# Optimization experiments

Measured on AMD Instinct MI355X. Metric: run time of the kernel, lower is better.

Reference implementation:

```python
import jax, jax.numpy as jnp
import numpy as np
from jax import lax

C = 256
K = 7
PAD = (K - 1) // 2
EMB = 128
MULT = 4
HID = C * MULT
B = 16
L = 4096
EPS = 1e-6
LAYER_SCALE_INIT = 1e-6


def setup_inputs() -> dict:
    key = jax.random.key(0)
    ks = jax.random.split(key, 10)
    x = jax.random.normal(ks[0], (B, C, L), dtype=jnp.float32)
    t = jax.random.normal(ks[1], (B, EMB), dtype=jnp.float32)
    # depthwise conv: Conv1d(C, C, K, groups=C) -> weight [C, 1, K]
    dw_w = jax.random.normal(ks[2], (C, 1, K), dtype=jnp.float32) * 0.1
    dw_b = jax.random.normal(ks[3], (C,), dtype=jnp.float32) * 0.02
    # FiLM linear: Linear(EMB, 2C)
    film_w = jax.random.normal(ks[4], (2 * C, EMB), dtype=jnp.float32) * 0.05
    film_b = jax.random.normal(ks[5], (2 * C,), dtype=jnp.float32) * 0.02
    # pointwise 1x1 convs
    pw1_w = jax.random.normal(ks[6], (HID, C), dtype=jnp.float32) * 0.05
    pw1_b = jax.random.normal(ks[7], (HID,), dtype=jnp.float32) * 0.02
    pw2_w = jax.random.normal(ks[8], (C, HID), dtype=jnp.float32) * 0.05
    pw2_b = jax.random.normal(ks[9], (C,), dtype=jnp.float32) * 0.02
    gamma = jnp.full((C, 1), LAYER_SCALE_INIT, dtype=jnp.float32)
    return {"x": x, "t": t, "dw_w": dw_w, "dw_b": dw_b,
            "film_w": film_w, "film_b": film_b,
            "pw1_w": pw1_w, "pw1_b": pw1_b,
            "pw2_w": pw2_w, "pw2_b": pw2_b, "gamma": gamma}


def reference(x, t, dw_w, dw_b, film_w, film_b, pw1_w, pw1_b, pw2_w, pw2_b, gamma):
    # circular pad on spatial dim, then valid depthwise conv
    xp = jnp.concatenate([x[..., -PAD:], x, x[..., :PAD]], axis=-1)  # [B, C, L+2*PAD]
    y = lax.conv_general_dilated(
        xp, dw_w, window_strides=(1,), padding='VALID',
        dimension_numbers=('NCH', 'OIH', 'NCH'),
        feature_group_count=C) + dw_b[:, None]                       # [B, C, L]
    # GroupNorm(1, C, affine=False): normalize over (C, L) per sample
    mu = jnp.mean(y, axis=(1, 2), keepdims=True)
    var = jnp.mean(jnp.square(y - mu), axis=(1, 2), keepdims=True)
    yn = (y - mu) * lax.rsqrt(var + EPS)
    # FiLM: scale/shift from embedded time
    ss = t @ film_w.T + film_b                                       # [B, 2C]
    scale, shift = jnp.split(ss, 2, axis=1)                          # [B, C] each
    yn = yn * (scale[:, :, None] + 1.0) + shift[:, :, None]
    # pointwise mixing with ReLU
    h = jax.nn.relu(jnp.einsum('bcl,dc->bdl', yn, pw1_w) + pw1_b[:, None])  # [B, HID, L]
    branch = jnp.einsum('bdl,cd->bcl', h, pw2_w) + pw2_b[:, None]           # [B, C, L]
    # layerscale + residual
    return x + branch * gamma
```

## Files before the change

kernel.cpp:

```cpp
#include <hip/hip_runtime.h>

typedef short s16x8 __attribute__((ext_vector_type(8)));
typedef short s16x4 __attribute__((ext_vector_type(4)));
typedef float f32x4 __attribute__((ext_vector_type(4)));

#define NB 16
#define NC 256
#define NL 4096
#define NH 1024
#define NE 128

#define WS_YNT   0ull
#define WS_PW1   33554432ull
#define WS_PW2   34078720ull
#define WS_AF    34603008ull
#define WS_BF    34619392ull

#define MFMA16(a, b, c) __builtin_amdgcn_mfma_f32_16x16x32_bf16((a), (b), (c), 0, 0, 0)

static __device__ __forceinline__ short f2bf(float f) {
    unsigned int u = __float_as_uint(f);
    u = (u + 0x7fffu + ((u >> 16) & 1u)) >> 16;
    return (short)u;
}
static __device__ __forceinline__ float bf2f(short s) {
    return __uint_as_float(((unsigned int)(unsigned short)s) << 16);
}

__global__ __launch_bounds__(256) void k0_prep(const float4* __restrict__ pw1,
                                               const float4* __restrict__ pw2,
                                               s16x4* __restrict__ pw1b,
                                               s16x4* __restrict__ pw2b) {
    const int idx = blockIdx.x * 256 + threadIdx.x;
    const float4 a = pw1[idx];
    const float4 b = pw2[idx];
    s16x4 oa, ob;
    oa[0] = f2bf(a.x); oa[1] = f2bf(a.y); oa[2] = f2bf(a.z); oa[3] = f2bf(a.w);
    ob[0] = f2bf(b.x); ob[1] = f2bf(b.y); ob[2] = f2bf(b.z); ob[3] = f2bf(b.w);
    pw1b[idx] = oa;
    pw2b[idx] = ob;
}

__global__ __launch_bounds__(256) void k1_dwconv(const float* __restrict__ x,
                                                 const float* __restrict__ dw_w,
                                                 const float* __restrict__ dw_b,
                                                 short* __restrict__ ynt,
                                                 float2* __restrict__ psum) {
    __shared__ float xt[64][81];
    __shared__ float red1[4], red2[4];
    const int b = blockIdx.x >> 8;
    const int rem = blockIdx.x & 255;
    const int c0 = (rem >> 6) << 6;
    const int l0 = (rem & 63) << 6;
    const int t = threadIdx.x;

    const float* xb = x + ((size_t)(b * NC + c0)) * NL;
    {
#pragma unroll
        for (int j = 0; j < 5; ++j) {
            const int idx = t + 256 * j;
            const int row = idx / 20;
            const int col = idx - row * 20;
            const int lg = (l0 - 4 + col * 4) & (NL - 1);
            const float4 v = *(const float4*)(xb + (size_t)row * NL + lg);
            xt[row][col * 4 + 0] = v.x;
            xt[row][col * 4 + 1] = v.y;
            xt[row][col * 4 + 2] = v.z;
            xt[row][col * 4 + 3] = v.w;
        }
    }

    const int c = t & 63;
    const int w = t >> 6;
    const float w0 = dw_w[(c0 + c) * 7 + 0], w1 = dw_w[(c0 + c) * 7 + 1],
                w2 = dw_w[(c0 + c) * 7 + 2], w3 = dw_w[(c0 + c) * 7 + 3],
                w4 = dw_w[(c0 + c) * 7 + 4], w5 = dw_w[(c0 + c) * 7 + 5],
                w6 = dw_w[(c0 + c) * 7 + 6];
    const float bb = dw_b[c0 + c];
    __syncthreads();

    float win0 = xt[c][w * 16 + 1], win1 = xt[c][w * 16 + 2], win2 = xt[c][w * 16 + 3],
          win3 = xt[c][w * 16 + 4], win4 = xt[c][w * 16 + 5], win5 = xt[c][w * 16 + 6],
          win6 = xt[c][w * 16 + 7];
    float s1 = 0.f, s2 = 0.f;
    short* yo = ynt + ((size_t)(b * NL + l0 + w * 16)) * NC + c0 + c;
#pragma unroll
    for (int i = 0; i < 16; ++i) {
        const float y = bb + w0 * win0 + w1 * win1 + w2 * win2 + w3 * win3 +
                        w4 * win4 + w5 * win5 + w6 * win6;
        s1 += y;
        s2 += y * y;
        yo[(size_t)i * NC] = f2bf(y);
        win0 = win1; win1 = win2; win2 = win3; win3 = win4; win4 = win5; win5 = win6;
        win6 = xt[c][w * 16 + i + 8];
    }
    for (int off = 32; off; off >>= 1) {
        s1 += __shfl_down(s1, off, 64);
        s2 += __shfl_down(s2, off, 64);
    }
    if ((t & 63) == 0) { red1[w] = s1; red2[w] = s2; }
    __syncthreads();
    if (t == 0) {
        psum[blockIdx.x] = make_float2(red1[0] + red1[1] + red1[2] + red1[3],
                                       red2[0] + red2[1] + red2[2] + red2[3]);
    }
}

__global__ __launch_bounds__(256) void k2_finalize(const float* __restrict__ tin,
                                                   const float* __restrict__ fw,
                                                   const float* __restrict__ fb,
                                                   const float2* __restrict__ psum,
                                                   float* __restrict__ afilm,
                                                   float* __restrict__ bfilm) {
    __shared__ float r1[4], r2[4];
    const int b = blockIdx.x;
    const int c = threadIdx.x;

    const float2 v = psum[b * 256 + c];
    float s1 = v.x, s2 = v.y;
    for (int off = 32; off; off >>= 1) {
        s1 += __shfl_down(s1, off, 64);
        s2 += __shfl_down(s2, off, 64);
    }
    if ((c & 63) == 0) { r1[c >> 6] = s1; r2[c >> 6] = s2; }
    __syncthreads();
    const float sum1 = r1[0] + r1[1] + r1[2] + r1[3];
    const float sum2 = r2[0] + r2[1] + r2[2] + r2[3];

    const float n = (float)(NC * NL);
    const float mu = sum1 / n;
    const float var = sum2 / n - mu * mu;
    const float rs = rsqrtf(var + 1e-6f);

    const f32x4* tv = (const f32x4*)(tin + b * NE);
    const f32x4* wA = (const f32x4*)(fw + (size_t)c * NE);
    const f32x4* wB = (const f32x4*)(fw + (size_t)(NC + c) * NE);
    float sc = 0.f, sh = 0.f;
#pragma unroll
    for (int e = 0; e < NE / 4; ++e) {
        f32x4 tq = tv[e], aq = wA[e], bq = wB[e];
        sc += tq[0] * aq[0] + tq[1] * aq[1] + tq[2] * aq[2] + tq[3] * aq[3];
        sh += tq[0] * bq[0] + tq[1] * bq[1] + tq[2] * bq[2] + tq[3] * bq[3];
    }
    sc += fb[c];
    sh += fb[NC + c];
    const float A = rs * (1.f + sc);
    afilm[b * NC + c] = A;
    bfilm[b * NC + c] = sh - mu * A;
}

__global__ __launch_bounds__(256, 2) void k3_gemm(
    const short* __restrict__ ynt, const short* __restrict__ pw1b,
    const short* __restrict__ pw2b, const float* __restrict__ pb1,
    const float* __restrict__ pb2, const float* __restrict__ afilm,
    const float* __restrict__ bfilm, const float* __restrict__ gamma,
    const float* __restrict__ x, float* __restrict__ out, int b0) {
    __shared__ short yn[64 * 264];
    __shared__ short hs[2][64 * 136];

    const int b = (blockIdx.x >> 6) + b0;
    const int l0 = (blockIdx.x & 63) << 6;
    const int t = threadIdx.x;
    const int lane = t & 63, wid = t >> 6;
    const int ln = lane & 15, quad = lane >> 4;

    {
        const int c8 = (t & 31) * 8;
        const int lrow = t >> 5;
        const f32x4 a0 = *(const f32x4*)(afilm + b * NC + c8);
        const f32x4 a1 = *(const f32x4*)(afilm + b * NC + c8 + 4);
        const f32x4 f0 = *(const f32x4*)(bfilm + b * NC + c8);
        const f32x4 f1 = *(const f32x4*)(bfilm + b * NC + c8 + 4);
        const short* ys = ynt + ((size_t)(b * NL + l0)) * NC + c8;
#pragma unroll
        for (int p = 0; p < 8; ++p) {
            const int l = p * 8 + lrow;
            s16x8 v = *(const s16x8*)(ys + (size_t)l * NC);
            s16x8 o;
#pragma unroll
            for (int j = 0; j < 4; ++j) {
                o[j]     = f2bf(a0[j] * bf2f(v[j])     + f0[j]);
                o[4 + j] = f2bf(a1[j] * bf2f(v[4 + j]) + f1[j]);
            }
            *(s16x8*)(yn + l * 264 + c8) = o;
        }
    }

    const short* A1b = pw1b + (size_t)(32 * wid + ln) * NC + quad * 8;
    const short* A2b = pw2b + (size_t)(64 * wid + ln) * NH + quad * 8;

    s16x8 a1p[16];
#pragma unroll
    for (int kk = 0; kk < 4; ++kk) {
        a1p[2 * kk + 0] = *(const s16x8*)(A1b + kk * 32);
        a1p[2 * kk + 1] = *(const s16x8*)(A1b + 16 * NC + kk * 32);
    }
    __syncthreads();
#pragma unroll
    for (int kk = 4; kk < 8; ++kk) {
        a1p[2 * kk + 0] = *(const s16x8*)(A1b + kk * 32);
        a1p[2 * kk + 1] = *(const s16x8*)(A1b + 16 * NC + kk * 32);
    }

    s16x8 a2p[16];
#pragma unroll
    for (int kk = 0; kk < 4; ++kk) {
#pragma unroll
        for (int m = 0; m < 4; ++m) {
            a2p[4 * kk + m] = *(const s16x8*)(A2b + m * 16 * NH + kk * 32);
        }
    }

    f32x4 acc1[2][4] = {};
#pragma unroll
    for (int kk = 0; kk < 8; ++kk) {
        const int kq = kk * 32 + quad * 8;
        s16x8 b0v = *(const s16x8*)(yn + (0 * 16 + ln) * 264 + kq);
        s16x8 b1v = *(const s16x8*)(yn + (1 * 16 + ln) * 264 + kq);
        s16x8 b2v = *(const s16x8*)(yn + (2 * 16 + ln) * 264 + kq);
        s16x8 b3v = *(const s16x8*)(yn + (3 * 16 + ln) * 264 + kq);
        acc1[0][0] = MFMA16(a1p[2 * kk], b0v, acc1[0][0]);
        acc1[0][1] = MFMA16(a1p[2 * kk], b1v, acc1[0][1]);
        acc1[0][2] = MFMA16(a1p[2 * kk], b2v, acc1[0][2]);
        acc1[0][3] = MFMA16(a1p[2 * kk], b3v, acc1[0][3]);
        acc1[1][0] = MFMA16(a1p[2 * kk + 1], b0v, acc1[1][0]);
        acc1[1][1] = MFMA16(a1p[2 * kk + 1], b1v, acc1[1][1]);
        acc1[1][2] = MFMA16(a1p[2 * kk + 1], b2v, acc1[1][2]);
        acc1[1][3] = MFMA16(a1p[2 * kk + 1], b3v, acc1[1][3]);
    }

    f32x4 acc2[4][4] = {};

#pragma unroll 1
    for (int ch = 0; ch < 7; ++ch) {
        const int dc0 = ch * 128;
        short* hw = &hs[ch & 1][0];
#pragma unroll
        for (int mf = 0; mf < 2; ++mf) {
            const int dbase = 32 * wid + mf * 16 + quad * 4;
            const f32x4 b1v = *(const f32x4*)(pb1 + dc0 + dbase);
#pragma unroll
            for (int nf = 0; nf < 4; ++nf) {
                const int l = nf * 16 + ln;
                s16x4 hv;
#pragma unroll
                for (int r = 0; r < 4; ++r) {
                    hv[r] = f2bf(fmaxf(acc1[mf][nf][r] + b1v[r], 0.f));
                }
                *(s16x4*)(hw + l * 136 + dbase) = hv;
            }
        }
        __syncthreads();
        const short* A1n = A1b + (size_t)(dc0 + 128) * NC;
#pragma unroll
        for (int kk = 0; kk < 4; ++kk) {
            a1p[2 * kk + 0] = *(const s16x8*)(A1n + kk * 32);
            a1p[2 * kk + 1] = *(const s16x8*)(A1n + 16 * NC + kk * 32);
        }
        const short* hr = &hs[ch & 1][0];
#pragma unroll
        for (int kk = 0; kk < 4; ++kk) {
            const int kq = kk * 32 + quad * 8;
            s16x8 h0 = *(const s16x8*)(hr + (0 * 16 + ln) * 136 + kq);
            s16x8 h1 = *(const s16x8*)(hr + (1 * 16 + ln) * 136 + kq);
            s16x8 h2 = *(const s16x8*)(hr + (2 * 16 + ln) * 136 + kq);
            s16x8 h3 = *(const s16x8*)(hr + (3 * 16 + ln) * 136 + kq);
            acc2[0][0] = MFMA16(a2p[4 * kk + 0], h0, acc2[0][0]);
            acc2[0][1] = MFMA16(a2p[4 * kk + 0], h1, acc2[0][1]);
            acc2[0][2] = MFMA16(a2p[4 * kk + 0], h2, acc2[0][2]);
            acc2[0][3] = MFMA16(a2p[4 * kk + 0], h3, acc2[0][3]);
            acc2[1][0] = MFMA16(a2p[4 * kk + 1], h0, acc2[1][0]);
            acc2[1][1] = MFMA16(a2p[4 * kk + 1], h1, acc2[1][1]);
            acc2[1][2] = MFMA16(a2p[4 * kk + 1], h2, acc2[1][2]);
            acc2[1][3] = MFMA16(a2p[4 * kk + 1], h3, acc2[1][3]);
            acc2[2][0] = MFMA16(a2p[4 * kk + 2], h0, acc2[2][0]);
            acc2[2][1] = MFMA16(a2p[4 * kk + 2], h1, acc2[2][1]);
            acc2[2][2] = MFMA16(a2p[4 * kk + 2], h2, acc2[2][2]);
            acc2[2][3] = MFMA16(a2p[4 * kk + 2], h3, acc2[2][3]);
            acc2[3][0] = MFMA16(a2p[4 * kk + 3], h0, acc2[3][0]);
            acc2[3][1] = MFMA16(a2p[4 * kk + 3], h1, acc2[3][1]);
            acc2[3][2] = MFMA16(a2p[4 * kk + 3], h2, acc2[3][2]);
            acc2[3][3] = MFMA16(a2p[4 * kk + 3], h3, acc2[3][3]);
        }
#pragma unroll
        for (int kk = 4; kk < 8; ++kk) {
            a1p[2 * kk + 0] = *(const s16x8*)(A1n + kk * 32);
            a1p[2 * kk + 1] = *(const s16x8*)(A1n + 16 * NC + kk * 32);
        }
        {
            const short* A2n = A2b + dc0 + 128;
#pragma unroll
            for (int kk = 0; kk < 4; ++kk) {
#pragma unroll
                for (int m = 0; m < 4; ++m) {
                    a2p[4 * kk + m] = *(const s16x8*)(A2n + m * 16 * NH + kk * 32);
                }
            }
        }
#pragma unroll
        for (int i = 0; i < 2; ++i)
#pragma unroll
            for (int j = 0; j < 4; ++j) acc1[i][j] = (f32x4){0.f, 0.f, 0.f, 0.f};
#pragma unroll
        for (int kk = 0; kk < 8; ++kk) {
            const int kq = kk * 32 + quad * 8;
            s16x8 b0v = *(const s16x8*)(yn + (0 * 16 + ln) * 264 + kq);
            s16x8 b1v = *(const s16x8*)(yn + (1 * 16 + ln) * 264 + kq);
            s16x8 b2v = *(const s16x8*)(yn + (2 * 16 + ln) * 264 + kq);
            s16x8 b3v = *(const s16x8*)(yn + (3 * 16 + ln) * 264 + kq);
            acc1[0][0] = MFMA16(a1p[2 * kk], b0v, acc1[0][0]);
            acc1[0][1] = MFMA16(a1p[2 * kk], b1v, acc1[0][1]);
            acc1[0][2] = MFMA16(a1p[2 * kk], b2v, acc1[0][2]);
            acc1[0][3] = MFMA16(a1p[2 * kk], b3v, acc1[0][3]);
            acc1[1][0] = MFMA16(a1p[2 * kk + 1], b0v, acc1[1][0]);
            acc1[1][1] = MFMA16(a1p[2 * kk + 1], b1v, acc1[1][1]);
            acc1[1][2] = MFMA16(a1p[2 * kk + 1], b2v, acc1[1][2]);
            acc1[1][3] = MFMA16(a1p[2 * kk + 1], b3v, acc1[1][3]);
        }
    }

    {
        short* hw = &hs[1][0];
#pragma unroll
        for (int mf = 0; mf < 2; ++mf) {
            const int dbase = 32 * wid + mf * 16 + quad * 4;
            const f32x4 b1v = *(const f32x4*)(pb1 + 7 * 128 + dbase);
#pragma unroll
            for (int nf = 0; nf < 4; ++nf) {
                const int l = nf * 16 + ln;
                s16x4 hv;
#pragma unroll
                for (int r = 0; r < 4; ++r) {
                    hv[r] = f2bf(fmaxf(acc1[mf][nf][r] + b1v[r], 0.f));
                }
                *(s16x4*)(hw + l * 136 + dbase) = hv;
            }
        }
        __syncthreads();
        const short* hr = &hs[1][0];
#pragma unroll
        for (int kk = 0; kk < 4; ++kk) {
            const int kq = kk * 32 + quad * 8;
            s16x8 h0 = *(const s16x8*)(hr + (0 * 16 + ln) * 136 + kq);
            s16x8 h1 = *(const s16x8*)(hr + (1 * 16 + ln) * 136 + kq);
            s16x8 h2 = *(const s16x8*)(hr + (2 * 16 + ln) * 136 + kq);
            s16x8 h3 = *(const s16x8*)(hr + (3 * 16 + ln) * 136 + kq);
            acc2[0][0] = MFMA16(a2p[4 * kk + 0], h0, acc2[0][0]);
            acc2[0][1] = MFMA16(a2p[4 * kk + 0], h1, acc2[0][1]);
            acc2[0][2] = MFMA16(a2p[4 * kk + 0], h2, acc2[0][2]);
            acc2[0][3] = MFMA16(a2p[4 * kk + 0], h3, acc2[0][3]);
            acc2[1][0] = MFMA16(a2p[4 * kk + 1], h0, acc2[1][0]);
            acc2[1][1] = MFMA16(a2p[4 * kk + 1], h1, acc2[1][1]);
            acc2[1][2] = MFMA16(a2p[4 * kk + 1], h2, acc2[1][2]);
            acc2[1][3] = MFMA16(a2p[4 * kk + 1], h3, acc2[1][3]);
            acc2[2][0] = MFMA16(a2p[4 * kk + 2], h0, acc2[2][0]);
            acc2[2][1] = MFMA16(a2p[4 * kk + 2], h1, acc2[2][1]);
            acc2[2][2] = MFMA16(a2p[4 * kk + 2], h2, acc2[2][2]);
            acc2[2][3] = MFMA16(a2p[4 * kk + 2], h3, acc2[2][3]);
            acc2[3][0] = MFMA16(a2p[4 * kk + 3], h0, acc2[3][0]);
            acc2[3][1] = MFMA16(a2p[4 * kk + 3], h1, acc2[3][1]);
            acc2[3][2] = MFMA16(a2p[4 * kk + 3], h2, acc2[3][2]);
            acc2[3][3] = MFMA16(a2p[4 * kk + 3], h3, acc2[3][3]);
        }
    }

#pragma unroll
    for (int mf2 = 0; mf2 < 4; ++mf2) {
        const int cbase = 64 * wid + mf2 * 16 + quad * 4;
        const f32x4 g4 = *(const f32x4*)(gamma + cbase);
        const f32x4 b4 = *(const f32x4*)(pb2 + cbase);
#pragma unroll
        for (int r = 0; r < 4; ++r) {
            const int c = cbase + r;
            const size_t base = ((size_t)(b * NC + c)) * NL + l0 + ln;
            const float* xr = x + base;
            float* orow = out + base;
#pragma unroll
            for (int nf2 = 0; nf2 < 4; ++nf2) {
                orow[nf2 * 16] = xr[nf2 * 16] + g4[r] * (acc2[mf2][nf2][r] + b4[r]);
            }
        }
    }
}

extern "C" void kernel_launch(void* const* d_in, const int* in_sizes, int n_in,
                              void* d_out, int out_size, void* d_ws, size_t ws_size,
                              hipStream_t stream) {
    (void)in_sizes; (void)n_in; (void)out_size; (void)ws_size;
    const float* x      = (const float*)d_in[0];
    const float* tin    = (const float*)d_in[1];
    const float* dw_w   = (const float*)d_in[2];
    const float* dw_b   = (const float*)d_in[3];
    const float* film_w = (const float*)d_in[4];
    const float* film_b = (const float*)d_in[5];
    const float* pw1_w  = (const float*)d_in[6];
    const float* pw1_b  = (const float*)d_in[7];
    const float* pw2_w  = (const float*)d_in[8];
    const float* pw2_b  = (const float*)d_in[9];
    const float* gamma  = (const float*)d_in[10];
    float* out = (float*)d_out;

    char* ws = (char*)d_ws;
    short* ynt  = (short*)(ws + WS_YNT);
    short* pw1b = (short*)(ws + WS_PW1);
    short* pw2b = (short*)(ws + WS_PW2);
    float* afilm = (float*)(ws + WS_AF);
    float* bfilm = (float*)(ws + WS_BF);
    float2* psum = (float2*)d_out;

    hipLaunchKernelGGL(k0_prep, dim3(256), dim3(256), 0, stream,
                       (const float4*)pw1_w, (const float4*)pw2_w,
                       (s16x4*)pw1b, (s16x4*)pw2b);
    hipLaunchKernelGGL(k1_dwconv, dim3(NB * 256), dim3(256), 0, stream,
                       x, dw_w, dw_b, ynt, psum);
    hipLaunchKernelGGL(k2_finalize, dim3(NB), dim3(256), 0, stream,
                       tin, film_w, film_b, psum, afilm, bfilm);
    hipLaunchKernelGGL(k3_gemm, dim3((NB / 4) * (NL / 64)), dim3(256), 0, stream,
                       ynt, pw1b, pw2b, pw1_b, pw2_b, afilm, bfilm, gamma, x, out, 0);
    hipLaunchKernelGGL(k3_gemm, dim3((NB / 4) * (NL / 64)), dim3(256), 0, stream,
                       ynt, pw1b, pw2b, pw1_b, pw2_b, afilm, bfilm, gamma, x, out, 4);
    hipLaunchKernelGGL(k3_gemm, dim3((NB / 4) * (NL / 64)), dim3(256), 0, stream,
                       ynt, pw1b, pw2b, pw1_b, pw2_b, afilm, bfilm, gamma, x, out, 8);
    hipLaunchKernelGGL(k3_gemm, dim3((NB / 4) * (NL / 64)), dim3(256), 0, stream,
                       ynt, pw1b, pw2b, pw1_b, pw2_b, afilm, bfilm, gamma, x, out, 12);
}
```

Measured before the change: 323.3 us.

## Fuse weight prep into dwconv and FiLM finalize into GEMM, single GEMM launch

Merges the bf16 weight conversion into the depthwise-conv kernel as extra blocks. It moves the GroupNorm/FiLM finalize into the start of every GEMM block, so each block recomputes the per-sample scale and shift into shared memory. The four per-batch-chunk GEMM launches become one launch over all batches, and psum moves from the output buffer into the workspace. This cuts the launch count from seven to two and removes the serial tiny finalize kernel. The cost is redundant FiLM dot products and reductions in each of the 1024 GEMM blocks, plus slightly more shared memory.

```diff
diff --git a/kernel.cpp b/kernel.cpp
--- a/kernel.cpp
+++ b/kernel.cpp
@@ -13,8 +13,7 @@
 #define WS_YNT   0ull
 #define WS_PW1   33554432ull
 #define WS_PW2   34078720ull
-#define WS_AF    34603008ull
-#define WS_BF    34619392ull
+#define WS_PSUM  34603008ull
 
 #define MFMA16(a, b, c) __builtin_amdgcn_mfma_f32_16x16x32_bf16((a), (b), (c), 0, 0, 0)
 
@@ -27,32 +26,35 @@
     return __uint_as_float(((unsigned int)(unsigned short)s) << 16);
 }
 
-__global__ __launch_bounds__(256) void k0_prep(const float4* __restrict__ pw1,
-                                               const float4* __restrict__ pw2,
-                                               s16x4* __restrict__ pw1b,
-                                               s16x4* __restrict__ pw2b) {
-    const int idx = blockIdx.x * 256 + threadIdx.x;
-    const float4 a = pw1[idx];
-    const float4 b = pw2[idx];
-    s16x4 oa, ob;
-    oa[0] = f2bf(a.x); oa[1] = f2bf(a.y); oa[2] = f2bf(a.z); oa[3] = f2bf(a.w);
-    ob[0] = f2bf(b.x); ob[1] = f2bf(b.y); ob[2] = f2bf(b.z); ob[3] = f2bf(b.w);
-    pw1b[idx] = oa;
-    pw2b[idx] = ob;
-}
-
-__global__ __launch_bounds__(256) void k1_dwconv(const float* __restrict__ x,
+__global__ __launch_bounds__(256) void k01_fused(const float* __restrict__ x,
                                                  const float* __restrict__ dw_w,
                                                  const float* __restrict__ dw_b,
                                                  short* __restrict__ ynt,
-                                                 float2* __restrict__ psum) {
+                                                 float2* __restrict__ psum,
+                                                 const float4* __restrict__ pw1,
+                                                 const float4* __restrict__ pw2,
+                                                 s16x4* __restrict__ pw1b,
+                                                 s16x4* __restrict__ pw2b) {
     __shared__ float xt[64][81];
     __shared__ float red1[4], red2[4];
+    const int t = threadIdx.x;
+
+    if (blockIdx.x >= NB * 256) {
+        const int idx = (blockIdx.x - NB * 256) * 256 + t;
+        const float4 a = pw1[idx];
+        const float4 bq = pw2[idx];
+        s16x4 oa, ob;
+        oa[0] = f2bf(a.x); oa[1] = f2bf(a.y); oa[2] = f2bf(a.z); oa[3] = f2bf(a.w);
+        ob[0] = f2bf(bq.x); ob[1] = f2bf(bq.y); ob[2] = f2bf(bq.z); ob[3] = f2bf(bq.w);
+        pw1b[idx] = oa;
+        pw2b[idx] = ob;
+        return;
+    }
+
     const int b = blockIdx.x >> 8;
     const int rem = blockIdx.x & 255;
     const int c0 = (rem >> 6) << 6;
     const int l0 = (rem & 63) << 6;
-    const int t = threadIdx.x;
 
     const float* xb = x + ((size_t)(b * NC + c0)) * NL;
     {
@@ -106,71 +108,65 @@
     }
 }
 
-__global__ __launch_bounds__(256) void k2_finalize(const float* __restrict__ tin,
-                                                   const float* __restrict__ fw,
-                                                   const float* __restrict__ fb,
-                                                   const float2* __restrict__ psum,
-                                                   float* __restrict__ afilm,
-                                                   float* __restrict__ bfilm) {
-    __shared__ float r1[4], r2[4];
-    const int b = blockIdx.x;
-    const int c = threadIdx.x;
-
-    const float2 v = psum[b * 256 + c];
-    float s1 = v.x, s2 = v.y;
-    for (int off = 32; off; off >>= 1) {
-        s1 += __shfl_down(s1, off, 64);
-        s2 += __shfl_down(s2, off, 64);
-    }
-    if ((c & 63) == 0) { r1[c >> 6] = s1; r2[c >> 6] = s2; }
-    __syncthreads();
-    const float sum1 = r1[0] + r1[1] + r1[2] + r1[3];
-    const float sum2 = r2[0] + r2[1] + r2[2] + r2[3];
-
-    const float n = (float)(NC * NL);
-    const float mu = sum1 / n;
-    const float var = sum2 / n - mu * mu;
-    const float rs = rsqrtf(var + 1e-6f);
-
-    const f32x4* tv = (const f32x4*)(tin + b * NE);
-    const f32x4* wA = (const f32x4*)(fw + (size_t)c * NE);
-    const f32x4* wB = (const f32x4*)(fw + (size_t)(NC + c) * NE);
-    float sc = 0.f, sh = 0.f;
-#pragma unroll
-    for (int e = 0; e < NE / 4; ++e) {
-        f32x4 tq = tv[e], aq = wA[e], bq = wB[e];
-        sc += tq[0] * aq[0] + tq[1] * aq[1] + tq[2] * aq[2] + tq[3] * aq[3];
-        sh += tq[0] * bq[0] + tq[1] * bq[1] + tq[2] * bq[2] + tq[3] * bq[3];
-    }
-    sc += fb[c];
-    sh += fb[NC + c];
-    const float A = rs * (1.f + sc);
-    afilm[b * NC + c] = A;
-    bfilm[b * NC + c] = sh - mu * A;
-}
-
 __global__ __launch_bounds__(256, 2) void k3_gemm(
     const short* __restrict__ ynt, const short* __restrict__ pw1b,
     const short* __restrict__ pw2b, const float* __restrict__ pb1,
-    const float* __restrict__ pb2, const float* __restrict__ afilm,
-    const float* __restrict__ bfilm, const float* __restrict__ gamma,
-    const float* __restrict__ x, float* __restrict__ out, int b0) {
+    const float* __restrict__ pb2, const float* __restrict__ tin,
+    const float* __restrict__ fw, const float* __restrict__ fb,
+    const float2* __restrict__ psum, const float* __restrict__ gamma,
+    const float* __restrict__ x, float* __restrict__ out) {
     __shared__ short yn[64 * 264];
     __shared__ short hs[2][64 * 136];
-
-    const int b = (blockIdx.x >> 6) + b0;
+    __shared__ float afs[NC], bfs[NC];
+    __shared__ float r1[4], r2[4];
+
+    const int b = blockIdx.x >> 6;
     const int l0 = (blockIdx.x & 63) << 6;
     const int t = threadIdx.x;
     const int lane = t & 63, wid = t >> 6;
     const int ln = lane & 15, quad = lane >> 4;
 
     {
+        const float2 v = psum[b * 256 + t];
+        float s1 = v.x, s2 = v.y;
+        for (int off = 32; off; off >>= 1) {
+            s1 += __shfl_down(s1, off, 64);
+            s2 += __shfl_down(s2, off, 64);
+        }
+        if ((t & 63) == 0) { r1[t >> 6] = s1; r2[t >> 6] = s2; }
+        __syncthreads();
+        const float sum1 = r1[0] + r1[1] + r1[2] + r1[3];
+        const float sum2 = r2[0] + r2[1] + r2[2] + r2[3];
+        const float n = (float)(NC * NL);
+        const float mu = sum1 / n;
+        const float var = sum2 / n - mu * mu;
+        const float rs = rsqrtf(var + 1e-6f);
+
+        const f32x4* tv = (const f32x4*)(tin + b * NE);
+        const f32x4* wA = (const f32x4*)(fw + (size_t)t * NE);
+        const f32x4* wB = (const f32x4*)(fw + (size_t)(NC + t) * NE);
+        float sc = 0.f, sh = 0.f;
+#pragma unroll
+        for (int e = 0; e < NE / 4; ++e) {
+            f32x4 tq = tv[e], aq = wA[e], bq = wB[e];
+            sc += tq[0] * aq[0] + tq[1] * aq[1] + tq[2] * aq[2] + tq[3] * aq[3];
+            sh += tq[0] * bq[0] + tq[1] * bq[1] + tq[2] * bq[2] + tq[3] * bq[3];
+        }
+        sc += fb[t];
+        sh += fb[NC + t];
+        const float A = rs * (1.f + sc);
+        afs[t] = A;
+        bfs[t] = sh - mu * A;
+        __syncthreads();
+    }
+
+    {
         const int c8 = (t & 31) * 8;
         const int lrow = t >> 5;
-        const f32x4 a0 = *(const f32x4*)(afilm + b * NC + c8);
-        const f32x4 a1 = *(const f32x4*)(afilm + b * NC + c8 + 4);
-        const f32x4 f0 = *(const f32x4*)(bfilm + b * NC + c8);
-        const f32x4 f1 = *(const f32x4*)(bfilm + b * NC + c8 + 4);
+        const f32x4 a0 = *(const f32x4*)(afs + c8);
+        const f32x4 a1 = *(const f32x4*)(afs + c8 + 4);
+        const f32x4 f0 = *(const f32x4*)(bfs + c8);
+        const f32x4 f1 = *(const f32x4*)(bfs + c8 + 4);
         const short* ys = ynt + ((size_t)(b * NL + l0)) * NC + c8;
 #pragma unroll
         for (int p = 0; p < 8; ++p) {
@@ -404,23 +400,13 @@
     short* ynt  = (short*)(ws + WS_YNT);
     short* pw1b = (short*)(ws + WS_PW1);
     short* pw2b = (short*)(ws + WS_PW2);
-    float* afilm = (float*)(ws + WS_AF);
-    float* bfilm = (float*)(ws + WS_BF);
-    float2* psum = (float2*)d_out;
-
-    hipLaunchKernelGGL(k0_prep, dim3(256), dim3(256), 0, stream,
+    float2* psum = (float2*)(ws + WS_PSUM);
+
+    hipLaunchKernelGGL(k01_fused, dim3(NB * 256 + 256), dim3(256), 0, stream,
+                       x, dw_w, dw_b, ynt, psum,
                        (const float4*)pw1_w, (const float4*)pw2_w,
                        (s16x4*)pw1b, (s16x4*)pw2b);
-    hipLaunchKernelGGL(k1_dwconv, dim3(NB * 256), dim3(256), 0, stream,
-                       x, dw_w, dw_b, ynt, psum);
-    hipLaunchKernelGGL(k2_finalize, dim3(NB), dim3(256), 0, stream,
-                       tin, film_w, film_b, psum, afilm, bfilm);
-    hipLaunchKernelGGL(k3_gemm, dim3((NB / 4) * (NL / 64)), dim3(256), 0, stream,
-                       ynt, pw1b, pw2b, pw1_b, pw2_b, afilm, bfilm, gamma, x, out, 0);
-    hipLaunchKernelGGL(k3_gemm, dim3((NB / 4) * (NL / 64)), dim3(256), 0, stream,
-                       ynt, pw1b, pw2b, pw1_b, pw2_b, afilm, bfilm, gamma, x, out, 4);
-    hipLaunchKernelGGL(k3_gemm, dim3((NB / 4) * (NL / 64)), dim3(256), 0, stream,
-                       ynt, pw1b, pw2b, pw1_b, pw2_b, afilm, bfilm, gamma, x, out, 8);
-    hipLaunchKernelGGL(k3_gemm, dim3((NB / 4) * (NL / 64)), dim3(256), 0, stream,
-                       ynt, pw1b, pw2b, pw1_b, pw2_b, afilm, bfilm, gamma, x, out, 12);
+    hipLaunchKernelGGL(k3_gemm, dim3(NB * (NL / 64)), dim3(256), 0, stream,
+                       ynt, pw1b, pw2b, pw1_b, pw2_b, tin, film_w, film_b,
+                       psum, gamma, x, out);
 }
```

Result: faster. 299.8 us (-7.3%).
